# Kernel optimization log

Hardware: AMD Instinct MI355X
Metric: run time of the kernel (lower is better)

Reference implementation:

```python
import jax, jax.numpy as jnp
import numpy as np

N_NODES = 50000
N_EDGES = 800000
D_IN, D_HID, D_OUT = 128, 512, 128


def setup_inputs() -> dict:
    key = jax.random.key(0)
    k1, k2, k3, k4, k5 = jax.random.split(key, 5)
    nh = jax.random.normal(k1, (N_NODES, D_IN), dtype=jnp.float32)
    eh = jax.random.normal(k2, (N_EDGES, D_IN), dtype=jnp.float32)
    edge_index = jax.random.randint(k3, (2, N_EDGES), 0, N_NODES, dtype=jnp.int64)
    # 2-layer GIN MLP params (Linear(128->512), relu, Linear(512->128)), bias=True
    W1 = jax.random.normal(k4, (D_IN, D_HID), dtype=jnp.float32) * (1.0 / np.sqrt(D_IN))
    b1 = jnp.zeros((D_HID,), dtype=jnp.float32)
    W2 = jax.random.normal(k5, (D_HID, D_OUT), dtype=jnp.float32) * (1.0 / np.sqrt(D_HID))
    b2 = jnp.zeros((D_OUT,), dtype=jnp.float32)
    eps = jnp.zeros((1,), dtype=jnp.float32)  # nf_eps parameter, init 0.0
    return {"nh": nh, "eh": eh, "W1": W1, "b1": b1, "W2": W2, "b2": b2,
            "eps": eps, "edge_index": edge_index}


def reference(nh, eh, W1, b1, W2, b2, eps, edge_index):
    src, dst = edge_index[0], edge_index[1]
    # gather src features, scatter-add into dst nodes: [N, D_IN]
    nz = jax.ops.segment_sum(nh[src], dst, num_segments=nh.shape[0])
    n_h = (1.0 + eps) * nh + nz  # epsilon-scaled residual
    # GIN MLP: Linear -> relu -> Linear (dropout=0, eval)
    h = jax.nn.relu(jnp.einsum("nd,dh->nh", n_h, W1) + b1)
    n_h = jnp.einsum("nh,ho->no", h, W2) + b2
    return (n_h, eh)
```

## Files before the change

kernel.cpp:

```cpp
#include <hip/hip_runtime.h>

#define N_NODES 50000
#define N_EDGES 800000
#define D_IN 128
#define D_HID 512
#define D_OUT 128

#define EH_FLOAT4 (N_EDGES * (D_IN / 4))
#define CPB 4096

#define C_PREP 400
#define C_HIST 450
#define C_SCAN 200
#define C_FILL 450
#define C_GATH 1200
#define C_GEMM1 1900
#define C_GEMM2 1650

typedef __attribute__((ext_vector_type(8))) short short8v;
typedef __attribute__((ext_vector_type(4))) float f32x4;

__device__ __forceinline__ unsigned short f2bf(float f) {
    union { float f; unsigned u; } v; v.f = f;
    unsigned u = v.u;
    return (unsigned short)((u + 0x7FFFu + ((u >> 16) & 1u)) >> 16);
}
__device__ __forceinline__ float bf2f(unsigned u16) {
    union { unsigned u; float f; } v; v.u = u16 << 16;
    return v.f;
}

__device__ __forceinline__ long long interleave(long long b, long long C,
                                                long long T, long long* w) {
    long long cb = (C == 0) ? 0 : (b * C) / T;
    bool isCopy = C != 0 && ((b + 1) * C) / T > cb;
    *w = b - cb;
    return isCopy ? cb : -1;
}

__device__ __forceinline__ void copy_chunk(const float4* __restrict__ src,
                                           float4* __restrict__ dst,
                                           long long base, long long cb) {
    const f32x4* s = (const f32x4*)src;
    f32x4* d = (f32x4*)dst;
    long long o = base + cb * CPB + threadIdx.x;
#pragma unroll
    for (int i = 0; i < 16; ++i) {
        f32x4 v = __builtin_nontemporal_load(&s[o + i * 256]);
        __builtin_nontemporal_store(v, &d[o + i * 256]);
    }
}

__global__ __launch_bounds__(256) void k_prep(const float4* __restrict__ nh,
                                              const float* __restrict__ W1,
                                              const float* __restrict__ W2,
                                              uint2* __restrict__ nh16,
                                              unsigned short* __restrict__ W1T,
                                              unsigned short* __restrict__ W2T,
                                              int* __restrict__ counts,
                                              int* __restrict__ pub,
                                              const float4* __restrict__ csrc,
                                              float4* __restrict__ cdst,
                                              long long copyBase, int copyC) {
    long long w;
    const int W = 6250 + 256 + 256 + 196;
    long long cb = interleave(blockIdx.x, copyC, W + copyC, &w);
    if (cb >= 0) { copy_chunk(csrc, cdst, copyBase, cb); return; }
    int tid = threadIdx.x;
    if (w < 6250) {
        int i = (int)w * 256 + tid;
        if (i < N_NODES * (D_IN / 4)) {
            float4 a = nh[i];
            uint2 r;
            r.x = (unsigned)f2bf(a.x) | ((unsigned)f2bf(a.y) << 16);
            r.y = (unsigned)f2bf(a.z) | ((unsigned)f2bf(a.w) << 16);
            nh16[i] = r;
        }
    } else if (w < 6506) {
        int i = (int)(w - 6250) * 256 + tid;
        int n = i >> 7, k = i & 127;
        W1T[i] = f2bf(W1[k * D_HID + n]);
    } else if (w < 6762) {
        int i = (int)(w - 6506) * 256 + tid;
        int n = i >> 9, k = i & 511;
        W2T[i] = f2bf(W2[k * D_OUT + n]);
    } else {
        int i = (int)(w - 6762) * 256 + tid;
        if (i <= N_NODES) counts[i] = 0;
        if (i < 196) pub[i] = 0;
    }
}


__global__ __launch_bounds__(256) void k_hist(const int* __restrict__ ei,
                                              int* __restrict__ counts,
                                              const float4* __restrict__ csrc,
                                              float4* __restrict__ cdst,
                                              long long copyBase, int copyC) {
    long long w;
    const int W = (N_EDGES + 255) / 256;
    long long cb = interleave(blockIdx.x, copyC, W + copyC, &w);
    if (cb >= 0) { copy_chunk(csrc, cdst, copyBase, cb); return; }
    int e = (int)w * 256 + threadIdx.x;
    if (e >= N_EDGES) return;
    atomicAdd(&counts[ei[N_EDGES + e]], 1);
}

__global__ __launch_bounds__(256) void k_scan_lb(const int* __restrict__ counts,
                                                 int* __restrict__ offs,
                                                 int* __restrict__ cursors,
                                                 int* __restrict__ pub,
                                                 const float4* __restrict__ csrc,
                                                 float4* __restrict__ cdst,
                                                 long long copyBase, int copyC) {
    long long w;
    long long cb = interleave(blockIdx.x, copyC, 196 + copyC, &w);
    if (cb >= 0) { copy_chunk(csrc, cdst, copyBase, cb); return; }
    int b = (int)w;
    __shared__ int s[256];
    __shared__ int r[256];
    int tid = threadIdx.x;
    int i = b * 256 + tid;
    int v = (i < N_NODES) ? counts[i] : 0;
    s[tid] = v;
    __syncthreads();
#pragma unroll
    for (int off = 1; off < 256; off <<= 1) {
        int t = (tid >= off) ? s[tid - off] : 0;
        __syncthreads();
        if (tid >= off) s[tid] += t;
        __syncthreads();
    }
    if (tid == 255)
        __hip_atomic_store(&pub[b], s[255] + 1, __ATOMIC_RELEASE,
                           __HIP_MEMORY_SCOPE_AGENT);
    int contrib = 0;
    if (tid < b) {
        int p;
        do {
            p = __hip_atomic_load(&pub[tid], __ATOMIC_ACQUIRE,
                                  __HIP_MEMORY_SCOPE_AGENT);
        } while (p == 0);
        contrib = p - 1;
    }
    r[tid] = contrib;
    __syncthreads();
#pragma unroll
    for (int off = 128; off > 0; off >>= 1) {
        if (tid < off) r[tid] += r[tid + off];
        __syncthreads();
    }
    int prefix = r[0];
    if (i < N_NODES) {
        int o = (s[tid] - v) + prefix;
        offs[i] = o;
        cursors[i] = o;
    }
    if (b == 0 && tid == 0) offs[N_NODES] = N_EDGES;
}

__global__ __launch_bounds__(256) void k_fill(const int* __restrict__ ei,
                                              int* __restrict__ cursors,
                                              int* __restrict__ csr_src,
                                              const float4* __restrict__ csrc,
                                              float4* __restrict__ cdst,
                                              long long copyBase, int copyC) {
    long long w;
    const int W = (N_EDGES + 255) / 256;
    long long cb = interleave(blockIdx.x, copyC, W + copyC, &w);
    if (cb >= 0) { copy_chunk(csrc, cdst, copyBase, cb); return; }
    int e = (int)w * 256 + threadIdx.x;
    if (e >= N_EDGES) return;
    int dst = ei[N_EDGES + e];
    int pos = atomicAdd(&cursors[dst], 1);
    csr_src[pos] = ei[e];
}

__global__ __launch_bounds__(256) void k_gather16(const unsigned* __restrict__ nh16,
                                                  const int* __restrict__ csr_src,
                                                  const int* __restrict__ offs,
                                                  const float* __restrict__ eps,
                                                  unsigned* __restrict__ acc16,
                                                  const float4* __restrict__ csrc,
                                                  float4* __restrict__ cdst,
                                                  long long copyBase, int copyC) {
    long long w;
    const int W = (N_NODES + 3) / 4;
    long long cb = interleave(blockIdx.x, copyC, W + copyC, &w);
    if (cb >= 0) { copy_chunk(csrc, cdst, copyBase, cb); return; }
    int node = (int)w * 4 + (threadIdx.x >> 6);
    if (node >= N_NODES) return;
    int lane = threadIdx.x & 63;
    int beg = offs[node], end = offs[node + 1];
    float sx = 0.f, sy = 0.f;
    int j = beg;
    for (; j + 1 < end; j += 2) {
        unsigned v0 = nh16[(size_t)csr_src[j] * 64 + lane];
        unsigned v1 = nh16[(size_t)csr_src[j + 1] * 64 + lane];
        sx += bf2f(v0 & 0xFFFFu) + bf2f(v1 & 0xFFFFu);
        sy += bf2f(v0 >> 16) + bf2f(v1 >> 16);
    }
    if (j < end) {
        unsigned v0 = nh16[(size_t)csr_src[j] * 64 + lane];
        sx += bf2f(v0 & 0xFFFFu);
        sy += bf2f(v0 >> 16);
    }
    float sc = 1.0f + eps[0];
    unsigned m = nh16[(size_t)node * 64 + lane];
    sx += sc * bf2f(m & 0xFFFFu);
    sy += sc * bf2f(m >> 16);
    acc16[(size_t)node * 64 + lane] =
        (unsigned)f2bf(sx) | ((unsigned)f2bf(sy) << 16);
}

__global__ __launch_bounds__(256) void k_copy_eh(const float4* __restrict__ src,
                                                 float4* __restrict__ dst) {
    int i = blockIdx.x * 256 + threadIdx.x;
    if (i >= EH_FLOAT4) return;
    const f32x4* s = (const f32x4*)src;
    f32x4* d = (f32x4*)dst;
    f32x4 v = __builtin_nontemporal_load(&s[i]);
    __builtin_nontemporal_store(v, &d[i]);
}

template <bool RELU, bool OUTBF16>
__global__ __launch_bounds__(256) void gemm_mfma(const unsigned short* __restrict__ A,
                                                 const unsigned short* __restrict__ Bt,
                                                 const float* __restrict__ bias,
                                                 void* __restrict__ Cout,
                                                 int M, int N, int K, int nx,
                                                 const float4* __restrict__ csrc,
                                                 float4* __restrict__ cdst,
                                                 long long copyBase, int copyC,
                                                 int workW) {
    long long w;
    long long cb = interleave(blockIdx.x, copyC, workW + copyC, &w);
    if (cb >= 0) { copy_chunk(csrc, cdst, copyBase, cb); return; }

    __shared__ unsigned short As[128][40];
    __shared__ unsigned short Bs[128][40];

    const int tid = threadIdx.x;
    const int m0 = ((int)w / nx) * 128;
    const int n0 = ((int)w % nx) * 128;
    const int wid = tid >> 6;
    const int lane = tid & 63;
    const int wr = wid >> 1;
    const int wc = wid & 1;
    const int l15 = lane & 15;
    const int kg = lane >> 4;

    f32x4 acc[4][4];
#pragma unroll
    for (int i = 0; i < 4; ++i)
#pragma unroll
        for (int j = 0; j < 4; ++j) acc[i][j] = (f32x4){0.f, 0.f, 0.f, 0.f};

    for (int k0 = 0; k0 < K; k0 += 32) {
#pragma unroll
        for (int p = 0; p < 2; ++p) {
            int t = tid + p * 256;
            int row = t >> 2;
            int cg = t & 3;
            float4 va = make_float4(0.f, 0.f, 0.f, 0.f);
            int gr = m0 + row;
            if (gr < M) va = *(const float4*)(A + (size_t)gr * K + k0 + cg * 8);
            *(float4*)&As[row][cg * 8] = va;
            float4 vb = *(const float4*)(Bt + (size_t)(n0 + row) * K + k0 + cg * 8);
            *(float4*)&Bs[row][cg * 8] = vb;
        }
        __syncthreads();

        short8v a[4], bb[4];
#pragma unroll
        for (int i = 0; i < 4; ++i)
            a[i] = *(const short8v*)&As[wr * 64 + i * 16 + l15][kg * 8];
#pragma unroll
        for (int j = 0; j < 4; ++j)
            bb[j] = *(const short8v*)&Bs[wc * 64 + j * 16 + l15][kg * 8];
#pragma unroll
        for (int i = 0; i < 4; ++i)
#pragma unroll
            for (int j = 0; j < 4; ++j)
                acc[i][j] = __builtin_amdgcn_mfma_f32_16x16x32_bf16(
                    a[i], bb[j], acc[i][j], 0, 0, 0);
        __syncthreads();
    }

    const int rbase = (lane >> 4) * 4;
#pragma unroll
    for (int j = 0; j < 4; ++j) {
        int gc = n0 + wc * 64 + j * 16 + l15;
        float bv = bias[gc];
#pragma unroll
        for (int i = 0; i < 4; ++i) {
#pragma unroll
            for (int q = 0; q < 4; ++q) {
                int gr = m0 + wr * 64 + i * 16 + rbase + q;
                if (gr >= M) continue;
                float v = acc[i][j][q] + bv;
                if (RELU) v = fmaxf(v, 0.f);
                if (OUTBF16)
                    ((unsigned short*)Cout)[(size_t)gr * N + gc] = f2bf(v);
                else
                    ((float*)Cout)[(size_t)gr * N + gc] = v;
            }
        }
    }
}

extern "C" void kernel_launch(void* const* d_in, const int* in_sizes, int n_in,
                              void* d_out, int out_size, void* d_ws, size_t ws_size,
                              hipStream_t stream) {
    const float* nh  = (const float*)d_in[0];
    const float* eh  = (const float*)d_in[1];
    const float* W1  = (const float*)d_in[2];
    const float* b1  = (const float*)d_in[3];
    const float* W2  = (const float*)d_in[4];
    const float* b2  = (const float*)d_in[5];
    const float* eps = (const float*)d_in[6];
    const int*   ei  = (const int*)d_in[7];

    float* out0 = (float*)d_out;
    float* out1 = out0 + (size_t)N_NODES * D_OUT;

    const size_t NEED = 88u << 20;
    bool useWs = (d_ws != nullptr) && (ws_size >= NEED);
    char* base = useWs ? (char*)d_ws : (char*)out1;

    unsigned*       nh16  = (unsigned*)(base);
    unsigned*       acc16 = (unsigned*)(base + (13u << 20));
    unsigned short* h16   = (unsigned short*)(base + (26u << 20));
    unsigned short* w1t   = (unsigned short*)(base + (78u << 20));
    unsigned short* w2t   = (unsigned short*)(base + (79u << 20));
    int*            ibase = (int*)(base + (80u << 20));
    int* offs    = ibase;
    int* cursors = ibase + 65536;
    int* pub     = ibase + 131072;
    int* csr_src = ibase + 262144;

    const float4* csrc = (const float4*)eh;
    float4*       cdst = (float4*)out1;

    int c0 = useWs ? C_PREP  : 0;  long long b0 = 0;
    int c1 = useWs ? C_HIST  : 0;  long long b1c = (long long)(C_PREP) * CPB;
    int c2 = useWs ? C_SCAN  : 0;  long long b2c = (long long)(C_PREP + C_HIST) * CPB;
    int c3 = useWs ? C_FILL  : 0;  long long b3c = (long long)(C_PREP + C_HIST + C_SCAN) * CPB;
    int c4 = useWs ? C_GATH  : 0;  long long b4c = (long long)(C_PREP + C_HIST + C_SCAN + C_FILL) * CPB;
    int c5 = useWs ? C_GEMM1 : 0;  long long b5c = (long long)(C_PREP + C_HIST + C_SCAN + C_FILL + C_GATH) * CPB;
    int c6 = useWs ? C_GEMM2 : 0;  long long b6c = b5c + (long long)C_GEMM1 * CPB;

    k_prep<<<6958 + c0, 256, 0, stream>>>((const float4*)nh, W1, W2,
        (uint2*)nh16, w1t, w2t, cursors, pub, csrc, cdst, b0, c0);

    k_hist<<<3125 + c1, 256, 0, stream>>>(ei, cursors, csrc, cdst, b1c, c1);
    k_scan_lb<<<196 + c2, 256, 0, stream>>>(cursors, offs, cursors, pub,
                                            csrc, cdst, b2c, c2);
    k_fill<<<3125 + c3, 256, 0, stream>>>(ei, cursors, csr_src, csrc, cdst, b3c, c3);
    k_gather16<<<12500 + c4, 256, 0, stream>>>(nh16, csr_src, offs, eps, acc16,
                                               csrc, cdst, b4c, c4);

    const int W1blocks = (D_HID / 128) * ((N_NODES + 127) / 128);
    const int W2blocks = (D_OUT / 128) * ((N_NODES + 127) / 128);
    gemm_mfma<true, true><<<W1blocks + c5, 256, 0, stream>>>(
        (const unsigned short*)acc16, w1t, b1, (void*)h16,
        N_NODES, D_HID, D_IN, D_HID / 128, csrc, cdst, b5c, c5, W1blocks);
    gemm_mfma<false, false><<<W2blocks + c6, 256, 0, stream>>>(
        h16, w2t, b2, (void*)out0,
        N_NODES, D_OUT, D_HID, D_OUT / 128, csrc, cdst, b6c, c6, W2blocks);

    if (!useWs) {
        k_copy_eh<<<(EH_FLOAT4 + 255) / 256, 256, 0, stream>>>(csrc, cdst);
    }
}
```

Measured before the change: 337.9 us.

## Fuse both MLP GEMMs into one kernel keeping hidden activations in LDS

```diff
diff --git a/kernel.cpp b/kernel.cpp
--- a/kernel.cpp
+++ b/kernel.cpp
@@ -14,8 +14,7 @@
 #define C_SCAN 200
 #define C_FILL 450
 #define C_GATH 1200
-#define C_GEMM1 1900
-#define C_GEMM2 1650
+#define C_GEMMF 3550
 
 typedef __attribute__((ext_vector_type(8))) short short8v;
 typedef __attribute__((ext_vector_type(4))) float f32x4;
@@ -223,26 +222,26 @@
     __builtin_nontemporal_store(v, &d[i]);
 }
 
-template <bool RELU, bool OUTBF16>
-__global__ __launch_bounds__(256) void gemm_mfma(const unsigned short* __restrict__ A,
-                                                 const unsigned short* __restrict__ Bt,
-                                                 const float* __restrict__ bias,
-                                                 void* __restrict__ Cout,
-                                                 int M, int N, int K, int nx,
-                                                 const float4* __restrict__ csrc,
-                                                 float4* __restrict__ cdst,
-                                                 long long copyBase, int copyC,
-                                                 int workW) {
+__global__ __launch_bounds__(256, 2) void gemm_fused(
+        const unsigned short* __restrict__ A,
+        const unsigned short* __restrict__ W1t,
+        const float* __restrict__ b1,
+        const unsigned short* __restrict__ W2t,
+        const float* __restrict__ b2,
+        float* __restrict__ Cout,
+        int M,
+        const float4* __restrict__ csrc, float4* __restrict__ cdst,
+        long long copyBase, int copyC, int workW) {
     long long w;
     long long cb = interleave(blockIdx.x, copyC, workW + copyC, &w);
     if (cb >= 0) { copy_chunk(csrc, cdst, copyBase, cb); return; }
 
     __shared__ unsigned short As[128][40];
     __shared__ unsigned short Bs[128][40];
+    __shared__ unsigned short Hs[128][136];
 
     const int tid = threadIdx.x;
-    const int m0 = ((int)w / nx) * 128;
-    const int n0 = ((int)w % nx) * 128;
+    const int m0 = (int)w * 128;
     const int wid = tid >> 6;
     const int lane = tid & 63;
     const int wr = wid >> 1;
@@ -250,60 +249,96 @@
     const int l15 = lane & 15;
     const int kg = lane >> 4;
 
-    f32x4 acc[4][4];
+    f32x4 acc2[4][4];
 #pragma unroll
     for (int i = 0; i < 4; ++i)
 #pragma unroll
-        for (int j = 0; j < 4; ++j) acc[i][j] = (f32x4){0.f, 0.f, 0.f, 0.f};
-
-    for (int k0 = 0; k0 < K; k0 += 32) {
-#pragma unroll
-        for (int p = 0; p < 2; ++p) {
-            int t = tid + p * 256;
-            int row = t >> 2;
-            int cg = t & 3;
-            float4 va = make_float4(0.f, 0.f, 0.f, 0.f);
-            int gr = m0 + row;
-            if (gr < M) va = *(const float4*)(A + (size_t)gr * K + k0 + cg * 8);
-            *(float4*)&As[row][cg * 8] = va;
-            float4 vb = *(const float4*)(Bt + (size_t)(n0 + row) * K + k0 + cg * 8);
-            *(float4*)&Bs[row][cg * 8] = vb;
+        for (int j = 0; j < 4; ++j) acc2[i][j] = (f32x4){0.f, 0.f, 0.f, 0.f};
+
+    for (int ht = 0; ht < 4; ++ht) {
+        f32x4 acc1[4][4];
+#pragma unroll
+        for (int i = 0; i < 4; ++i)
+#pragma unroll
+            for (int j = 0; j < 4; ++j) acc1[i][j] = (f32x4){0.f, 0.f, 0.f, 0.f};
+
+        for (int ks = 0; ks < 4; ++ks) {
+#pragma unroll
+            for (int p = 0; p < 2; ++p) {
+                int t = tid + p * 256;
+                int row = t >> 2;
+                int cg = t & 3;
+                float4 va = make_float4(0.f, 0.f, 0.f, 0.f);
+                int gr = m0 + row;
+                if (gr < M)
+                    va = *(const float4*)(A + (size_t)gr * D_IN + ks * 32 + cg * 8);
+                *(float4*)&As[row][cg * 8] = va;
+                float4 vb = *(const float4*)(W1t + (size_t)(ht * 128 + row) * D_IN
+                                             + ks * 32 + cg * 8);
+                *(float4*)&Bs[row][cg * 8] = vb;
+            }
+            __syncthreads();
+            short8v a[4], bb[4];
+#pragma unroll
+            for (int i = 0; i < 4; ++i)
+                a[i] = *(const short8v*)&As[wr * 64 + i * 16 + l15][kg * 8];
+#pragma unroll
+            for (int j = 0; j < 4; ++j)
+                bb[j] = *(const short8v*)&Bs[wc * 64 + j * 16 + l15][kg * 8];
+#pragma unroll
+            for (int i = 0; i < 4; ++i)
+#pragma unroll
+                for (int j = 0; j < 4; ++j)
+                    acc1[i][j] = __builtin_amdgcn_mfma_f32_16x16x32_bf16(
+                        a[i], bb[j], acc1[i][j], 0, 0, 0);
+            __syncthreads();
+        }
+
+#pragma unroll
+        for (int j = 0; j < 4; ++j) {
+            int lc = wc * 64 + j * 16 + l15;
+            float bv = b1[ht * 128 + lc];
+#pragma unroll
+            for (int i = 0; i < 4; ++i)
+#pragma unroll
+                for (int q = 0; q < 4; ++q) {
+                    float v = acc1[i][j][q] + bv;
+                    Hs[wr * 64 + i * 16 + kg * 4 + q][lc] = f2bf(fmaxf(v, 0.f));
+                }
         }
         __syncthreads();
 
-        short8v a[4], bb[4];
-#pragma unroll
-        for (int i = 0; i < 4; ++i)
-            a[i] = *(const short8v*)&As[wr * 64 + i * 16 + l15][kg * 8];
-#pragma unroll
-        for (int j = 0; j < 4; ++j)
-            bb[j] = *(const short8v*)&Bs[wc * 64 + j * 16 + l15][kg * 8];
-#pragma unroll
-        for (int i = 0; i < 4; ++i)
+#pragma unroll
+        for (int ks = 0; ks < 4; ++ks) {
+            short8v a[4], bb[4];
+#pragma unroll
+            for (int i = 0; i < 4; ++i)
+                a[i] = *(const short8v*)&Hs[wr * 64 + i * 16 + l15][ks * 32 + kg * 8];
 #pragma unroll
             for (int j = 0; j < 4; ++j)
-                acc[i][j] = __builtin_amdgcn_mfma_f32_16x16x32_bf16(
-                    a[i], bb[j], acc[i][j], 0, 0, 0);
+                bb[j] = *(const short8v*)(W2t + (size_t)(wc * 64 + j * 16 + l15) * D_HID
+                                          + ht * 128 + ks * 32 + kg * 8);
+#pragma unroll
+            for (int i = 0; i < 4; ++i)
+#pragma unroll
+                for (int j = 0; j < 4; ++j)
+                    acc2[i][j] = __builtin_amdgcn_mfma_f32_16x16x32_bf16(
+                        a[i], bb[j], acc2[i][j], 0, 0, 0);
+        }
         __syncthreads();
     }
 
-    const int rbase = (lane >> 4) * 4;
 #pragma unroll
     for (int j = 0; j < 4; ++j) {
-        int gc = n0 + wc * 64 + j * 16 + l15;
-        float bv = bias[gc];
+        int gc = wc * 64 + j * 16 + l15;
+        float bv = b2[gc];
 #pragma unroll
         for (int i = 0; i < 4; ++i) {
 #pragma unroll
             for (int q = 0; q < 4; ++q) {
-                int gr = m0 + wr * 64 + i * 16 + rbase + q;
+                int gr = m0 + wr * 64 + i * 16 + kg * 4 + q;
                 if (gr >= M) continue;
-                float v = acc[i][j][q] + bv;
-                if (RELU) v = fmaxf(v, 0.f);
-                if (OUTBF16)
-                    ((unsigned short*)Cout)[(size_t)gr * N + gc] = f2bf(v);
-                else
-                    ((float*)Cout)[(size_t)gr * N + gc] = v;
+                Cout[(size_t)gr * D_OUT + gc] = acc2[i][j][q] + bv;
             }
         }
     }
@@ -324,16 +359,15 @@
     float* out0 = (float*)d_out;
     float* out1 = out0 + (size_t)N_NODES * D_OUT;
 
-    const size_t NEED = 88u << 20;
+    const size_t NEED = 36u << 20;
     bool useWs = (d_ws != nullptr) && (ws_size >= NEED);
     char* base = useWs ? (char*)d_ws : (char*)out1;
 
     unsigned*       nh16  = (unsigned*)(base);
     unsigned*       acc16 = (unsigned*)(base + (13u << 20));
-    unsigned short* h16   = (unsigned short*)(base + (26u << 20));
-    unsigned short* w1t   = (unsigned short*)(base + (78u << 20));
-    unsigned short* w2t   = (unsigned short*)(base + (79u << 20));
-    int*            ibase = (int*)(base + (80u << 20));
+    unsigned short* w1t   = (unsigned short*)(base + (26u << 20));
+    unsigned short* w2t   = (unsigned short*)(base + (27u << 20));
+    int*            ibase = (int*)(base + (28u << 20));
     int* offs    = ibase;
     int* cursors = ibase + 65536;
     int* pub     = ibase + 131072;
@@ -347,8 +381,7 @@
     int c2 = useWs ? C_SCAN  : 0;  long long b2c = (long long)(C_PREP + C_HIST) * CPB;
     int c3 = useWs ? C_FILL  : 0;  long long b3c = (long long)(C_PREP + C_HIST + C_SCAN) * CPB;
     int c4 = useWs ? C_GATH  : 0;  long long b4c = (long long)(C_PREP + C_HIST + C_SCAN + C_FILL) * CPB;
-    int c5 = useWs ? C_GEMM1 : 0;  long long b5c = (long long)(C_PREP + C_HIST + C_SCAN + C_FILL + C_GATH) * CPB;
-    int c6 = useWs ? C_GEMM2 : 0;  long long b6c = b5c + (long long)C_GEMM1 * CPB;
+    int c5 = useWs ? C_GEMMF : 0;  long long b5c = (long long)(C_PREP + C_HIST + C_SCAN + C_FILL + C_GATH) * CPB;
 
     k_prep<<<6958 + c0, 256, 0, stream>>>((const float4*)nh, W1, W2,
         (uint2*)nh16, w1t, w2t, cursors, pub, csrc, cdst, b0, c0);
@@ -360,14 +393,10 @@
     k_gather16<<<12500 + c4, 256, 0, stream>>>(nh16, csr_src, offs, eps, acc16,
                                                csrc, cdst, b4c, c4);
 
-    const int W1blocks = (D_HID / 128) * ((N_NODES + 127) / 128);
-    const int W2blocks = (D_OUT / 128) * ((N_NODES + 127) / 128);
-    gemm_mfma<true, true><<<W1blocks + c5, 256, 0, stream>>>(
-        (const unsigned short*)acc16, w1t, b1, (void*)h16,
-        N_NODES, D_HID, D_IN, D_HID / 128, csrc, cdst, b5c, c5, W1blocks);
-    gemm_mfma<false, false><<<W2blocks + c6, 256, 0, stream>>>(
-        h16, w2t, b2, (void*)out0,
-        N_NODES, D_OUT, D_HID, D_OUT / 128, csrc, cdst, b6c, c6, W2blocks);
+    const int WFblocks = (N_NODES + 127) / 128;
+    gemm_fused<<<WFblocks + c5, 256, 0, stream>>>(
+        (const unsigned short*)acc16, w1t, b1, w2t, b2, out0,
+        N_NODES, csrc, cdst, b5c, c5, WFblocks);
 
     if (!useWs) {
         k_copy_eh<<<(EH_FLOAT4 + 255) / 256, 256, 0, stream>>>(csrc, cdst);
```

Result: faster. 319.6 us (-5.4%).
